# Kernel tuning notes

Hardware: AMD Instinct MI355X
Metric: run time of the kernel (lower is better)

The kernel has to match this reference:

```python
import jax, jax.numpy as jnp
import numpy as np

SEG_T = 0.7      # segmentation_map_threshold
GAUSS_T = 0.7    # gaussian_segmentation_threshold
EPS = 1e-07
PI_APPROX = 3.14  # literal used in the original code


def setup_inputs() -> dict:
    key = jax.random.key(0)
    k1, k2 = jax.random.split(key)
    B, H, W = 2, 80, 80
    variance_map = jax.random.normal(k1, (B, 3, H, W), dtype=jnp.float32)
    segmentation_map = jax.random.uniform(k2, (B, 1, H, W), dtype=jnp.float32)
    return {"variance_map": variance_map, "segmentation_map": segmentation_map}


def _splat_single(var, seg):
    # var: [3,H,W], seg: [H,W]
    H, W = seg.shape
    mask = (seg > SEG_T).reshape(-1)                      # [P], P = H*W (candidate points)
    vh = jnp.square(var[0].reshape(-1))                   # variance_height^2
    vw = jnp.square(var[1].reshape(-1))                   # variance_width^2
    th = PI_APPROX * jax.nn.sigmoid(var[2].reshape(-1))
    s, c = jnp.sin(th), jnp.cos(th)
    a = c * c / (2 * vh + EPS) + s * s / (2 * vw + EPS)
    b = -2 * s * c / (4 * vh + EPS) + 2 * s * c / (4 * vw + EPS)
    cc = s * s / (2 * vh + EPS) + c * c / (2 * vw + EPS)
    p = jnp.arange(H * W)
    x = (p // W).astype(jnp.float32)                      # row coordinate of each point
    y = (p % W).astype(jnp.float32)                       # col coordinate of each point
    ig, jg = jnp.meshgrid(jnp.arange(H, dtype=jnp.float32),
                          jnp.arange(W, dtype=jnp.float32), indexing="ij")
    di = ig[None, :, :] - x[:, None, None] + EPS          # [P,H,W]
    dj = jg[None, :, :] - y[:, None, None] + EPS          # [P,H,W]
    g = jnp.exp(-(a[:, None, None] * di * di
                  + b[:, None, None] * 2.0 * di * dj
                  + cc[:, None, None] * dj * dj) + EPS)   # [P,H,W]
    # zero out gaussians from points below the segmentation threshold;
    # since exp(.) > 0, this exactly matches max over only the nonzero points
    g = jnp.where(mask[:, None, None], g, 0.0)
    gmax = jnp.max(g, axis=0)                             # [H,W]
    return (gmax >= GAUSS_T).astype(gmax.dtype) * gmax


def reference(variance_map, segmentation_map):
    out = jax.vmap(_splat_single)(variance_map, segmentation_map[:, 0])  # [B,H,W]
    return out[:, None, :, :]                                            # [B,1,H,W]
```

## Files before the change

kernel.cpp:

```cpp
#include <hip/hip_runtime.h>
#include <math.h>

#define HGT 80
#define WID 80
#define HW 6400
#define SEG_T 0.7f
#define GAUSS_T 0.7f
#define EPSF 1e-7f
#define PI_APPROX 3.14f
#define EXP_CLAMP 85.0f
#define QKEEP 0.5f

#define NTHR 512
#define NWV  8
#define NIT  13

__global__ void __launch_bounds__(NTHR)
fused_kernel(const float* __restrict__ var, const float* __restrict__ seg,
             float* __restrict__ out) {
    __shared__ float qred[NWV][64];

    const int tid  = threadIdx.x;
    const int lane = tid & 63;
    const int wv   = tid >> 6;
    const int t    = blockIdx.x;
    const int b    = blockIdx.y;
    const int ti = t / 10, tj = t - ti * 10;
    const int pr = ti * 8 + (lane >> 3);
    const int pc = tj * 8 + (lane & 7);
    const float fi = (float)pr, fj = (float)pc;
    const float ii = fi * fi, ij = fi * fj, jj = fj * fj;
    const float tr0 = (float)(ti * 8), tr1 = (float)(ti * 8 + 7);
    const float tc0 = (float)(tj * 8), tc1 = (float)(tj * 8 + 7);

    const float* vb = var + (size_t)b * 3 * HW;
    const float* sg = seg + (size_t)b * HW;

    float qmin = 3.0e38f;

    for (int c = 0; c < NIT; ++c) {
        const int p = c * NTHR + tid;
        bool m = false;
        if (p < HW) m = sg[p] > SEG_T;

        float C0, C1, C2, C3, C4, C5;
        bool keep = false;
        if (m) {
            float v0 = vb[p], v1 = vb[HW + p], v2 = vb[2 * HW + p];
            float vh = v0 * v0, vw = v1 * v1;
            float th = PI_APPROX * (1.0f / (1.0f + expf(-v2)));
            float sn = sinf(th), cs = cosf(th);
            float A  = cs * cs / (2.0f * vh + EPSF) + sn * sn / (2.0f * vw + EPSF);
            float Bb = -2.0f * sn * cs / (4.0f * vh + EPSF)
                     +  2.0f * sn * cs / (4.0f * vw + EPSF);
            float Cc = sn * sn / (2.0f * vh + EPSF) + cs * cs / (2.0f * vw + EPSF);
            float B2 = 2.0f * Bb;
            int rr = p / WID, ccol = p - rr * WID;
            float u = EPSF - (float)rr;
            float v = EPSF - (float)ccol;
            C0 = A;
            C1 = B2;
            C2 = Cc;
            C3 = 2.0f * A * u + B2 * v;
            C4 = B2 * u + 2.0f * Cc * v;
            C5 = A * u * u + B2 * u * v + Cc * v * v;
            float hm = 0.5f * (A - Cc), hb = 0.5f * B2;
            float lmin = 0.5f * (A + Cc) - sqrtf(hm * hm + hb * hb);
            float x = (float)rr, y = (float)ccol;
            float dx = fmaxf(0.0f, fmaxf(tr0 - x, x - tr1));
            float dy = fmaxf(0.0f, fmaxf(tc0 - y, y - tc1));
            float d2 = dx * dx + dy * dy;
            keep = (lmin * d2) <= QKEEP;
        }

        unsigned long long msk = __ballot(keep);
        while (msk) {
            int s = (int)__builtin_ctzll(msk);
            msk &= msk - 1;
            float c0 = __shfl(C0, s), c1 = __shfl(C1, s);
            float c2 = __shfl(C2, s), c3 = __shfl(C3, s);
            float c4 = __shfl(C4, s), c5 = __shfl(C5, s);
            float Q = fmaf(c0, ii,
                      fmaf(c1, ij,
                      fmaf(c2, jj,
                      fmaf(c3, fi,
                      fmaf(c4, fj, c5)))));
            qmin = fminf(qmin, Q);
        }
    }

    qred[wv][lane] = qmin;
    __syncthreads();
    if (wv == 0) {
        float m2 = qred[0][lane];
        #pragma unroll
        for (int w = 1; w < NWV; ++w) m2 = fminf(m2, qred[w][lane]);
        float g = expf(fminf(EPSF - m2, EXP_CLAMP));
        out[(size_t)b * HW + pr * WID + pc] = (g >= GAUSS_T) ? g : 0.0f;
    }
}

extern "C" void kernel_launch(void* const* d_in, const int* in_sizes, int n_in,
                              void* d_out, int out_size, void* d_ws, size_t ws_size,
                              hipStream_t stream) {
    const float* var = (const float*)d_in[0];
    const float* seg = (const float*)d_in[1];
    float* out = (float*)d_out;
    int B = in_sizes[1] / HW;
    dim3 grid(100, B);
    fused_kernel<<<grid, NTHR, 0, stream>>>(var, seg, out);
}
```

Baseline: 68.53 us.

## Replace gather-by-tile with point-centric scatter using atomicMin over bounded boxes

Switches from each output tile scanning all candidate points to each candidate point scattering its quadratic form into a bounding box derived from its minimum eigenvalue, using atomicMin on order-preserving float keys in a workspace. Small boxes are handled per-thread inline, while large boxes are queued in shared memory and processed cooperatively by the block. A memset and a finalize kernel convert keys to outputs. This is meant to remove the O(points×tiles) work, at the cost of three launches and atomic contention.

Result: slower. 73.91 us (+7.8%).

```diff
diff --git a/kernel.cpp b/kernel.cpp
--- a/kernel.cpp
+++ b/kernel.cpp
@@ -11,92 +11,123 @@
 #define EXP_CLAMP 85.0f
 #define QKEEP 0.5f
 
-#define NTHR 512
-#define NWV  8
-#define NIT  13
+#define STHR 256
+#define SMALL_CAP 100
 
-__global__ void __launch_bounds__(NTHR)
-fused_kernel(const float* __restrict__ var, const float* __restrict__ seg,
-             float* __restrict__ out) {
-    __shared__ float qred[NWV][64];
 
-    const int tid  = threadIdx.x;
-    const int lane = tid & 63;
-    const int wv   = tid >> 6;
-    const int t    = blockIdx.x;
-    const int b    = blockIdx.y;
-    const int ti = t / 10, tj = t - ti * 10;
-    const int pr = ti * 8 + (lane >> 3);
-    const int pc = tj * 8 + (lane & 7);
-    const float fi = (float)pr, fj = (float)pc;
-    const float ii = fi * fi, ij = fi * fj, jj = fj * fj;
-    const float tr0 = (float)(ti * 8), tr1 = (float)(ti * 8 + 7);
-    const float tc0 = (float)(tj * 8), tc1 = (float)(tj * 8 + 7);
+__device__ __forceinline__ unsigned qkey(float q) {
+    unsigned b = __float_as_uint(q);
+    return (q < 0.0f) ? ~b : (b | 0x80000000u);
+}
 
-    const float* vb = var + (size_t)b * 3 * HW;
-    const float* sg = seg + (size_t)b * HW;
+__global__ void __launch_bounds__(STHR) scatter_kernel(
+        const float* __restrict__ var, const float* __restrict__ seg,
+        unsigned* __restrict__ keys, int n) {
+    __shared__ int qn;
+    __shared__ float qc[STHR][6];
+    __shared__ int   qm[STHR][5];
+    if (threadIdx.x == 0) qn = 0;
+    __syncthreads();
 
-    float qmin = 3.0e38f;
+    const int g = blockIdx.x * STHR + threadIdx.x;
+    float C0 = 0, C1 = 0, C2 = 0, C3 = 0, C4 = 0, C5 = 0;
+    int r0 = 0, r1 = -1, c0 = 0, c1 = -1, b = 0;
+    bool inline_me = false;
 
-    for (int c = 0; c < NIT; ++c) {
-        const int p = c * NTHR + tid;
-        bool m = false;
-        if (p < HW) m = sg[p] > SEG_T;
-
-        float C0, C1, C2, C3, C4, C5;
-        bool keep = false;
-        if (m) {
-            float v0 = vb[p], v1 = vb[HW + p], v2 = vb[2 * HW + p];
-            float vh = v0 * v0, vw = v1 * v1;
-            float th = PI_APPROX * (1.0f / (1.0f + expf(-v2)));
-            float sn = sinf(th), cs = cosf(th);
-            float A  = cs * cs / (2.0f * vh + EPSF) + sn * sn / (2.0f * vw + EPSF);
-            float Bb = -2.0f * sn * cs / (4.0f * vh + EPSF)
-                     +  2.0f * sn * cs / (4.0f * vw + EPSF);
-            float Cc = sn * sn / (2.0f * vh + EPSF) + cs * cs / (2.0f * vw + EPSF);
-            float B2 = 2.0f * Bb;
-            int rr = p / WID, ccol = p - rr * WID;
-            float u = EPSF - (float)rr;
-            float v = EPSF - (float)ccol;
+    if (g < n) {
+        b = g / HW;
+        const int p = g - b * HW;
+        if (seg[(size_t)b * HW + p] > SEG_T) {
+            const float* vb = var + (size_t)b * 3 * HW;
+            const float v0 = vb[p], v1 = vb[HW + p], v2 = vb[2 * HW + p];
+            const float vh = v0 * v0, vw = v1 * v1;
+            const float th = PI_APPROX * (1.0f / (1.0f + expf(-v2)));
+            const float sn = sinf(th), cs = cosf(th);
+            const float A  = cs * cs / (2.0f * vh + EPSF) + sn * sn / (2.0f * vw + EPSF);
+            const float Bb = -2.0f * sn * cs / (4.0f * vh + EPSF)
+                           +  2.0f * sn * cs / (4.0f * vw + EPSF);
+            const float Cc = sn * sn / (2.0f * vh + EPSF) + cs * cs / (2.0f * vw + EPSF);
+            const float B2 = 2.0f * Bb;
+            const int rr = p / WID, cc = p - rr * WID;
+            const float u = EPSF - (float)rr;
+            const float v = EPSF - (float)cc;
             C0 = A;
             C1 = B2;
             C2 = Cc;
             C3 = 2.0f * A * u + B2 * v;
             C4 = B2 * u + 2.0f * Cc * v;
             C5 = A * u * u + B2 * u * v + Cc * v * v;
-            float hm = 0.5f * (A - Cc), hb = 0.5f * B2;
-            float lmin = 0.5f * (A + Cc) - sqrtf(hm * hm + hb * hb);
-            float x = (float)rr, y = (float)ccol;
-            float dx = fmaxf(0.0f, fmaxf(tr0 - x, x - tr1));
-            float dy = fmaxf(0.0f, fmaxf(tc0 - y, y - tc1));
-            float d2 = dx * dx + dy * dy;
-            keep = (lmin * d2) <= QKEEP;
-        }
-
-        unsigned long long msk = __ballot(keep);
-        while (msk) {
-            int s = (int)__builtin_ctzll(msk);
-            msk &= msk - 1;
-            float c0 = __shfl(C0, s), c1 = __shfl(C1, s);
-            float c2 = __shfl(C2, s), c3 = __shfl(C3, s);
-            float c4 = __shfl(C4, s), c5 = __shfl(C5, s);
-            float Q = fmaf(c0, ii,
-                      fmaf(c1, ij,
-                      fmaf(c2, jj,
-                      fmaf(c3, fi,
-                      fmaf(c4, fj, c5)))));
-            qmin = fminf(qmin, Q);
+            const float hm = 0.5f * (A - Cc), hb = 0.5f * B2;
+            const float lmin = 0.5f * (A + Cc) - sqrtf(hm * hm + hb * hb);
+            int ri = HGT - 1;
+            if (lmin > 0.0f) {
+                const float R = sqrtf(QKEEP / lmin);
+                if (R < (float)(HGT - 1)) ri = (int)R + 1;
+            }
+            r0 = max(rr - ri, 0); r1 = min(rr + ri, HGT - 1);
+            c0 = max(cc - ri, 0); c1 = min(cc + ri, WID - 1);
+            const int area = (r1 - r0 + 1) * (c1 - c0 + 1);
+            if (area <= SMALL_CAP) {
+                inline_me = true;
+            } else {
+                const int s = atomicAdd(&qn, 1);
+                qc[s][0] = C0; qc[s][1] = C1; qc[s][2] = C2;
+                qc[s][3] = C3; qc[s][4] = C4; qc[s][5] = C5;
+                qm[s][0] = r0; qm[s][1] = r1; qm[s][2] = c0; qm[s][3] = c1;
+                qm[s][4] = b;
+            }
         }
     }
 
-    qred[wv][lane] = qmin;
+    if (inline_me) {
+        unsigned* kb = keys + (size_t)b * HW;
+        for (int i = r0; i <= r1; ++i) {
+            const float fi = (float)i, ii = fi * fi;
+            for (int j = c0; j <= c1; ++j) {
+                const float fj = (float)j;
+                const float Q = fmaf(C0, ii,
+                                fmaf(C1, fi * fj,
+                                fmaf(C2, fj * fj,
+                                fmaf(C3, fi,
+                                fmaf(C4, fj, C5)))));
+                if (Q <= QKEEP) atomicMin(&kb[i * WID + j], qkey(Q));
+            }
+        }
+    }
+
     __syncthreads();
-    if (wv == 0) {
-        float m2 = qred[0][lane];
-        #pragma unroll
-        for (int w = 1; w < NWV; ++w) m2 = fminf(m2, qred[w][lane]);
-        float g = expf(fminf(EPSF - m2, EXP_CLAMP));
-        out[(size_t)b * HW + pr * WID + pc] = (g >= GAUSS_T) ? g : 0.0f;
+    const int nq = qn;
+    for (int s = 0; s < nq; ++s) {
+        const float d0 = qc[s][0], d1 = qc[s][1], d2 = qc[s][2],
+                    d3 = qc[s][3], d4 = qc[s][4], d5 = qc[s][5];
+        const int R0 = qm[s][0], R1 = qm[s][1], Cl = qm[s][2], Cr = qm[s][3];
+        const int bb = qm[s][4];
+        const int wbox = Cr - Cl + 1;
+        const int tot  = (R1 - R0 + 1) * wbox;
+        unsigned* kb = keys + (size_t)bb * HW;
+        for (int t = threadIdx.x; t < tot; t += STHR) {
+            const int i = R0 + t / wbox;
+            const int j = Cl + (t - (t / wbox) * wbox);
+            const float fi = (float)i, fj = (float)j;
+            const float Q = fmaf(d0, fi * fi,
+                            fmaf(d1, fi * fj,
+                            fmaf(d2, fj * fj,
+                            fmaf(d3, fi,
+                            fmaf(d4, fj, d5)))));
+            if (Q <= QKEEP) atomicMin(&kb[i * WID + j], qkey(Q));
+        }
+    }
+}
+
+__global__ void __launch_bounds__(256) finalize_kernel(
+        const unsigned* __restrict__ keys, float* __restrict__ out, int n) {
+    const int i = blockIdx.x * 256 + threadIdx.x;
+    if (i < n) {
+        const unsigned k = keys[i];
+        const unsigned bits = (k & 0x80000000u) ? (k & 0x7fffffffu) : ~k;
+        const float Q = __uint_as_float(bits);
+        const float gg = expf(fminf(EPSF - Q, EXP_CLAMP));
+        out[i] = (gg >= GAUSS_T) ? gg : 0.0f;
     }
 }
 
@@ -106,7 +137,11 @@
     const float* var = (const float*)d_in[0];
     const float* seg = (const float*)d_in[1];
     float* out = (float*)d_out;
-    int B = in_sizes[1] / HW;
-    dim3 grid(100, B);
-    fused_kernel<<<grid, NTHR, 0, stream>>>(var, seg, out);
+    const int B = in_sizes[1] / HW;
+    const int n = B * HW;
+    unsigned* keys = (unsigned*)d_ws;
+
+    hipMemsetAsync(keys, 0xFE, (size_t)n * sizeof(unsigned), stream);
+    scatter_kernel<<<dim3((n + STHR - 1) / STHR), STHR, 0, stream>>>(var, seg, keys, n);
+    finalize_kernel<<<dim3((n + 255) / 256), 256, 0, stream>>>(keys, out, n);
 }
```
